# Kernel optimization log

Hardware: AMD Instinct MI355X
Metric: run time of the kernel (lower is better)

The kernel has to match this reference:

```python
import jax, jax.numpy as jnp
import numpy as np

DIM = 128       # pair channel dim
HID = 128       # orign_dim (projection dim)
N = 384         # sequence length (square pair map)
B = 1
EPS = 1e-5


def layer_norm(x, w, b):
    m = jnp.mean(x, axis=-1, keepdims=True)
    v = jnp.mean(jnp.square(x - m), axis=-1, keepdims=True)
    return (x - m) * jax.lax.rsqrt(v + EPS) * w + b


def setup_inputs() -> dict:
    key = jax.random.key(0)
    ks = jax.random.split(key, 16)
    s = 0.02
    return {
        "x": jax.random.normal(ks[0], (B, N, N, DIM), jnp.float32),
        "norm_w": jnp.ones((DIM,), jnp.float32),
        "norm_b": jnp.zeros((DIM,), jnp.float32),
        "left_w": jax.random.normal(ks[1], (HID, DIM), jnp.float32) * s,
        "left_b": jnp.zeros((HID,), jnp.float32),
        "right_w": jax.random.normal(ks[2], (HID, DIM), jnp.float32) * s,
        "right_b": jnp.zeros((HID,), jnp.float32),
        # gates: module inits weight=0, bias=1; use small random weights + bias 1
        # to keep the same math while exercising nontrivial values
        "lgate_w": jax.random.normal(ks[3], (HID, DIM), jnp.float32) * s,
        "lgate_b": jnp.ones((HID,), jnp.float32),
        "rgate_w": jax.random.normal(ks[4], (HID, DIM), jnp.float32) * s,
        "rgate_b": jnp.ones((HID,), jnp.float32),
        "ogate_w": jax.random.normal(ks[5], (HID, DIM), jnp.float32) * s,
        "ogate_b": jnp.ones((HID,), jnp.float32),
        "ton_w": jnp.ones((HID,), jnp.float32),
        "ton_b": jnp.zeros((HID,), jnp.float32),
        "out_w": jax.random.normal(ks[6], (DIM, HID), jnp.float32) * s,
        "out_b": jnp.zeros((DIM,), jnp.float32),
    }


def reference(x, norm_w, norm_b, left_w, left_b, right_w, right_b,
              lgate_w, lgate_b, rgate_w, rgate_b, ogate_w, ogate_b,
              ton_w, ton_b, out_w, out_b):
    xn = layer_norm(x, norm_w, norm_b)                       # [B,N,N,D]
    lin = lambda w, b: jnp.einsum('bijd,ed->bije', xn, w) + b
    left = lin(left_w, left_b) * jax.nn.sigmoid(lin(lgate_w, lgate_b))
    right = lin(right_w, right_b) * jax.nn.sigmoid(lin(rgate_w, rgate_b))
    out_gate = jax.nn.sigmoid(lin(ogate_w, ogate_b))
    # ingoing mix: '... k j d, ... k i d -> ... i j d'
    out = jnp.einsum('bkjd,bkid->bijd', left, right)         # [B,N,N,H]
    out = layer_norm(out, ton_w, ton_b)
    out = jnp.einsum('bijh,dh->bijd', out, out_w) + out_b
    return out * out_gate
```

## Files before the change

### kernel.cpp

```cpp
#include <hip/hip_runtime.h>
#include <stdint.h>

typedef unsigned short u16;
typedef short bf16x8 __attribute__((ext_vector_type(8)));
typedef short bf16x4 __attribute__((ext_vector_type(4)));
typedef float f32x4 __attribute__((ext_vector_type(4)));

#define NN 384
#define DIMC 128
#define NPOS (NN*NN)
#define EPSV 1e-5f
#define LNS 136

__device__ __forceinline__ u16 f2b(float f){
  union { float f; uint32_t u; } v; v.f = f;
  return (u16)((v.u + 0x7FFFu + ((v.u >> 16) & 1u)) >> 16);
}
__device__ __forceinline__ float b2f(u16 h){
  union { uint32_t u; float f; } v; v.u = ((uint32_t)h) << 16;
  return v.f;
}
__device__ __forceinline__ float sigm(float z){
  return __builtin_amdgcn_rcpf(1.0f + __expf(-z));
}

__device__ __forceinline__ void glds16(const u16* g, u16* l){
  __builtin_amdgcn_global_load_lds((const __attribute__((address_space(1))) void*)(g),
                                   (__attribute__((address_space(3))) void*)(l), 16, 0, 0);
}

__global__ void wconv_k(const float* __restrict__ s0, const float* __restrict__ s1,
                        const float* __restrict__ s2, const float* __restrict__ s3,
                        const float* __restrict__ s4, const float* __restrict__ s5,
                        u16* __restrict__ dst){
  int bid = blockIdx.x;
  int m = bid >> 6;
  int off = ((bid & 63) << 8) + threadIdx.x;
  const float* src = s0;
  if (m==1) src=s1; else if (m==2) src=s2; else if (m==3) src=s3;
  else if (m==4) src=s4; else if (m==5) src=s5;
  dst[(m<<14) + off] = f2b(src[off]);
}

__global__ __launch_bounds__(256) void proj_k(
    const float* __restrict__ x, const float* __restrict__ nw, const float* __restrict__ nb,
    const u16* __restrict__ wb,
    const float* __restrict__ left_b, const float* __restrict__ lgate_b,
    const float* __restrict__ right_b, const float* __restrict__ rgate_b,
    const float* __restrict__ ogate_b,
    u16* __restrict__ Lp, u16* __restrict__ Rp, u16* __restrict__ gate)
{
  __shared__ u16 xn[64*LNS];
  const int tid = threadIdx.x, lane = tid & 63, wid = tid >> 6;
  const int bid = blockIdx.x;
  const int c = bid % NN, r0 = (bid / NN) * 64;
  const int l15 = lane & 15, lg = lane >> 4;

  {
    float4 w0 = *(const float4*)(nw + l15*8);
    float4 w1 = *(const float4*)(nw + l15*8 + 4);
    float4 bb0 = *(const float4*)(nb + l15*8);
    float4 bb1 = *(const float4*)(nb + l15*8 + 4);
    #pragma unroll
    for (int it = 0; it < 4; ++it){
      int p = wid*16 + it*4 + lg;
      const float* xp = x + ((size_t)(r0 + p)*NN + c)*DIMC + l15*8;
      float4 v0 = *(const float4*)xp;
      float4 v1 = *(const float4*)(xp + 4);
      float s  = (v0.x+v0.y)+(v0.z+v0.w)+((v1.x+v1.y)+(v1.z+v1.w));
      float sq = v0.x*v0.x+v0.y*v0.y+v0.z*v0.z+v0.w*v0.w
               + v1.x*v1.x+v1.y*v1.y+v1.z*v1.z+v1.w*v1.w;
      #pragma unroll
      for (int o = 8; o; o >>= 1){ s += __shfl_xor(s, o); sq += __shfl_xor(sq, o); }
      float mean = s * (1.0f/128.0f);
      float var  = sq * (1.0f/128.0f) - mean*mean;
      float inv  = rsqrtf(var + EPSV);
      bf16x8 o8;
      o8[0] = (short)f2b((v0.x - mean)*inv*w0.x + bb0.x);
      o8[1] = (short)f2b((v0.y - mean)*inv*w0.y + bb0.y);
      o8[2] = (short)f2b((v0.z - mean)*inv*w0.z + bb0.z);
      o8[3] = (short)f2b((v0.w - mean)*inv*w0.w + bb0.w);
      o8[4] = (short)f2b((v1.x - mean)*inv*w1.x + bb1.x);
      o8[5] = (short)f2b((v1.y - mean)*inv*w1.y + bb1.y);
      o8[6] = (short)f2b((v1.z - mean)*inv*w1.z + bb1.z);
      o8[7] = (short)f2b((v1.w - mean)*inv*w1.w + bb1.w);
      *(bf16x8*)(xn + p*LNS + l15*8) = o8;
    }
  }
  __syncthreads();

  const int kofs = lg * 8;
  const int wrow = (wid*32 + l15) * 128;
  const int xrowbase = l15 * LNS;

  #pragma unroll
  for (int pr = 0; pr < 2; ++pr){
    const u16* wV = wb + (pr*2 + 0)*16384;
    const u16* wG = wb + (pr*2 + 1)*16384;
    const float* bV = pr ? right_b : left_b;
    const float* bG = pr ? rgate_b : lgate_b;
    u16* dst = pr ? Rp : Lp;

    f32x4 aV[2][4], aG[2][4];
    #pragma unroll
    for (int n = 0; n < 2; ++n)
      #pragma unroll
      for (int pt = 0; pt < 4; ++pt){ aV[n][pt] = {0.f,0.f,0.f,0.f}; aG[n][pt] = {0.f,0.f,0.f,0.f}; }

    #pragma unroll
    for (int ks = 0; ks < 4; ++ks){
      bf16x8 xf[4];
      #pragma unroll
      for (int pt = 0; pt < 4; ++pt)
        xf[pt] = *(const bf16x8*)(xn + xrowbase + pt*16*LNS + ks*32 + kofs);
      #pragma unroll
      for (int n = 0; n < 2; ++n){
        bf16x8 wv = *(const bf16x8*)(wV + wrow + n*16*128 + ks*32 + kofs);
        bf16x8 wg = *(const bf16x8*)(wG + wrow + n*16*128 + ks*32 + kofs);
        #pragma unroll
        for (int pt = 0; pt < 4; ++pt){
          aV[n][pt] = __builtin_amdgcn_mfma_f32_16x16x32_bf16(wv, xf[pt], aV[n][pt], 0, 0, 0);
          aG[n][pt] = __builtin_amdgcn_mfma_f32_16x16x32_bf16(wg, xf[pt], aG[n][pt], 0, 0, 0);
        }
      }
    }
    #pragma unroll
    for (int n = 0; n < 2; ++n){
      int ebase = wid*32 + n*16 + lg*4;
      float4 bv4 = *(const float4*)(bV + ebase);
      float4 bg4 = *(const float4*)(bG + ebase);
      #pragma unroll
      for (int r = 0; r < 4; ++r){
        float bv = r==0?bv4.x : r==1?bv4.y : r==2?bv4.z : bv4.w;
        float bg = r==0?bg4.x : r==1?bg4.y : r==2?bg4.z : bg4.w;
        u16* base = dst + (size_t)(ebase + r)*NPOS + (size_t)c*NN + r0 + l15;
        #pragma unroll
        for (int pt = 0; pt < 4; ++pt){
          float v = (aV[n][pt][r] + bv) * sigm(aG[n][pt][r] + bg);
          base[pt*16] = f2b(v);
        }
      }
    }
  }

  {
    const u16* wO = wb + 4*16384;
    f32x4 aO[2][4];
    #pragma unroll
    for (int n = 0; n < 2; ++n)
      #pragma unroll
      for (int pt = 0; pt < 4; ++pt) aO[n][pt] = {0.f,0.f,0.f,0.f};

    #pragma unroll
    for (int ks = 0; ks < 4; ++ks){
      bf16x8 xf[4];
      #pragma unroll
      for (int pt = 0; pt < 4; ++pt)
        xf[pt] = *(const bf16x8*)(xn + xrowbase + pt*16*LNS + ks*32 + kofs);
      #pragma unroll
      for (int n = 0; n < 2; ++n){
        bf16x8 wo = *(const bf16x8*)(wO + wrow + n*16*128 + ks*32 + kofs);
        #pragma unroll
        for (int pt = 0; pt < 4; ++pt)
          aO[n][pt] = __builtin_amdgcn_mfma_f32_16x16x32_bf16(wo, xf[pt], aO[n][pt], 0, 0, 0);
      }
    }
    __syncthreads();
    #pragma unroll
    for (int n = 0; n < 2; ++n){
      int ebase = wid*32 + n*16 + lg*4;
      float4 bo4 = *(const float4*)(ogate_b + ebase);
      #pragma unroll
      for (int r = 0; r < 4; ++r){
        float bo = r==0?bo4.x : r==1?bo4.y : r==2?bo4.z : bo4.w;
        #pragma unroll
        for (int pt = 0; pt < 4; ++pt)
          xn[(pt*16 + l15)*LNS + ebase + r] = f2b(sigm(aO[n][pt][r] + bo));
      }
    }
    __syncthreads();
    #pragma unroll
    for (int it = 0; it < 4; ++it){
      int idx = tid + it*256;
      int p = idx >> 4, s = idx & 15;
      *(bf16x8*)(gate + ((size_t)(r0 + p)*NN + c)*DIMC + s*8) = *(const bf16x8*)(xn + p*LNS + s*8);
    }
  }
}

__global__ __launch_bounds__(256) void phase2_k(const u16* __restrict__ Rp, const u16* __restrict__ Lp,
                                                u16* __restrict__ outp){
  __shared__ u16 lds[17408];
  u16* At = lds;
  u16* Bt = lds + 8192;
  const int tid = threadIdx.x, lane = tid & 63, wid = tid >> 6;
  const int bid = blockIdx.x;
  const int d = bid / 9, tile = bid % 9;
  const int i0 = (tile/3)*128, j0 = (tile%3)*128;
  const u16* Rb = Rp + (size_t)d*NPOS;
  const u16* Lb = Lp + (size_t)d*NPOS;
  const int wm = wid >> 1, wn = wid & 1;
  const int iw = wm*64, jw = wn*64;
  const int l15 = lane & 15, lg = lane >> 4;
  const int rmask = l15 & 7;

  int srcoff[4];
  #pragma unroll
  for (int c = 0; c < 4; ++c){
    int idx = wid*256 + c*64 + lane;
    int row = idx >> 3, slot = idx & 7;
    srcoff[c] = row*NN + ((slot ^ (row & 7)) * 8);
  }

  f32x4 acc[4][4];
  #pragma unroll
  for (int m = 0; m < 4; ++m)
    #pragma unroll
    for (int n = 0; n < 4; ++n) acc[m][n] = {0.f,0.f,0.f,0.f};

  const u16* Rt0 = Rb + (size_t)i0*NN;
  const u16* Lt0 = Lb + (size_t)j0*NN;

  for (int k0 = 0; k0 < NN; k0 += 64){
    __syncthreads();
    #pragma unroll
    for (int c = 0; c < 4; ++c){
      glds16(Rt0 + k0 + srcoff[c], At + (wid*4 + c)*512);
      glds16(Lt0 + k0 + srcoff[c], Bt + (wid*4 + c)*512);
    }
    asm volatile("s_waitcnt vmcnt(0)" ::: "memory");
    __syncthreads();
    #pragma unroll
    for (int ks = 0; ks < 2; ++ks){
      int sl = ((ks*4 + lg) ^ rmask) * 8;
      bf16x8 af[4], bfr[4];
      #pragma unroll
      for (int m = 0; m < 4; ++m)
        af[m] = *(const bf16x8*)(At + (iw + m*16 + l15)*64 + sl);
      #pragma unroll
      for (int n = 0; n < 4; ++n)
        bfr[n] = *(const bf16x8*)(Bt + (jw + n*16 + l15)*64 + sl);
      #pragma unroll
      for (int m = 0; m < 4; ++m)
        #pragma unroll
        for (int n = 0; n < 4; ++n)
          acc[m][n] = __builtin_amdgcn_mfma_f32_16x16x32_bf16(af[m], bfr[n], acc[m][n], 0, 0, 0);
    }
  }

  __syncthreads();
  #pragma unroll
  for (int m = 0; m < 4; ++m)
    #pragma unroll
    for (int n = 0; n < 4; ++n)
      #pragma unroll
      for (int r = 0; r < 4; ++r)
        lds[(iw + m*16 + lg*4 + r)*136 + jw + n*16 + l15] = f2b(acc[m][n][r]);
  __syncthreads();
  u16* ob = outp + (size_t)d*NPOS;
  #pragma unroll
  for (int it = 0; it < 8; ++it){
    int idx = tid + it*256;
    int i = idx >> 4, s = idx & 15;
    *(bf16x8*)(ob + (size_t)(i0 + i)*NN + j0 + s*8) = *(const bf16x8*)(lds + i*136 + s*8);
  }
}

__global__ __launch_bounds__(256) void phase3_k(const u16* __restrict__ outp,
    const float* __restrict__ tonw, const float* __restrict__ tonb,
    const u16* __restrict__ wOut, const float* __restrict__ out_b,
    const u16* __restrict__ gate, float* __restrict__ out)
{
  __shared__ u16 xn2[64*132];
  __shared__ float reds[4][64], redq[4][64];
  __shared__ float marr[64], iarr[64];
  const int tid = threadIdx.x, lane = tid & 63, wid = tid >> 6;
  const int bid = blockIdx.x;
  const int i = bid % NN, j0 = (bid / NN) * 64;
  const int l15 = lane & 15, lg = lane >> 4;

  float rv[32];
  float s = 0.f, sq = 0.f;
  #pragma unroll
  for (int q = 0; q < 32; ++q){
    int h = wid*32 + q;
    float v = b2f(outp[(size_t)h*NPOS + (size_t)i*NN + j0 + lane]);
    rv[q] = v; s += v; sq += v*v;
  }
  reds[wid][lane] = s; redq[wid][lane] = sq;
  __syncthreads();
  if (tid < 64){
    float ts = reds[0][tid] + reds[1][tid] + reds[2][tid] + reds[3][tid];
    float tq = redq[0][tid] + redq[1][tid] + redq[2][tid] + redq[3][tid];
    float m  = ts * (1.f/128.f);
    float var = tq * (1.f/128.f) - m*m;
    marr[tid] = m; iarr[tid] = rsqrtf(var + EPSV);
  }
  __syncthreads();
  float m = marr[lane], inv = iarr[lane];
  #pragma unroll
  for (int q = 0; q < 32; ++q){
    int h = wid*32 + q;
    float v = (rv[q] - m)*inv*tonw[h] + tonb[h];
    xn2[lane*132 + h] = f2b(v);
  }
  __syncthreads();

  f32x4 acc[8];
  #pragma unroll
  for (int n = 0; n < 8; ++n) acc[n] = {0.f,0.f,0.f,0.f};
  const int row = wid*16 + l15;
  const int kofs = lg * 8;
  #pragma unroll
  for (int ks = 0; ks < 4; ++ks){
    const u16* ap = xn2 + row*132 + ks*32 + kofs;
    bf16x4 a0 = *(const bf16x4*)ap;
    bf16x4 a1 = *(const bf16x4*)(ap + 4);
    bf16x8 af = __builtin_shufflevector(a0, a1, 0,1,2,3,4,5,6,7);
    #pragma unroll
    for (int n = 0; n < 8; ++n){
      bf16x8 bm = *(const bf16x8*)(wOut + (n*16 + l15)*128 + ks*32 + kofs);
      acc[n] = __builtin_amdgcn_mfma_f32_16x16x32_bf16(af, bm, acc[n], 0, 0, 0);
    }
  }
  #pragma unroll
  for (int n = 0; n < 8; ++n){
    int dd = n*16 + l15;
    float bo = out_b[dd];
    #pragma unroll
    for (int r = 0; r < 4; ++r){
      int p = wid*16 + lg*4 + r;
      size_t base = ((size_t)i*NN + j0 + p)*DIMC + dd;
      float g = b2f(gate[base]);
      out[base] = (acc[n][r] + bo) * g;
    }
  }
}

extern "C" void kernel_launch(void* const* d_in, const int* in_sizes, int n_in,
                              void* d_out, int out_size, void* d_ws, size_t ws_size,
                              hipStream_t stream){
  const float* x       = (const float*)d_in[0];
  const float* norm_w  = (const float*)d_in[1];
  const float* norm_b  = (const float*)d_in[2];
  const float* left_w  = (const float*)d_in[3];
  const float* left_b  = (const float*)d_in[4];
  const float* right_w = (const float*)d_in[5];
  const float* right_b = (const float*)d_in[6];
  const float* lgate_w = (const float*)d_in[7];
  const float* lgate_b = (const float*)d_in[8];
  const float* rgate_w = (const float*)d_in[9];
  const float* rgate_b = (const float*)d_in[10];
  const float* ogate_w = (const float*)d_in[11];
  const float* ogate_b = (const float*)d_in[12];
  const float* ton_w   = (const float*)d_in[13];
  const float* ton_b   = (const float*)d_in[14];
  const float* out_w   = (const float*)d_in[15];
  const float* out_b   = (const float*)d_in[16];

  char* ws = (char*)d_ws;
  const size_t SZ = (size_t)NPOS * DIMC * sizeof(u16);
  u16* Lp   = (u16*)(ws);
  u16* Rp   = (u16*)(ws + SZ);
  u16* gate = (u16*)(ws + 2*SZ);
  u16* outp = (u16*)(ws + 3*SZ);
  u16* wb   = (u16*)(ws + 4*SZ);

  wconv_k<<<dim3(384), dim3(256), 0, stream>>>(left_w, lgate_w, right_w, rgate_w, ogate_w, out_w, wb);
  proj_k<<<dim3(2304), dim3(256), 0, stream>>>(x, norm_w, norm_b, wb,
      left_b, lgate_b, right_b, rgate_b, ogate_b, Lp, Rp, gate);
  phase2_k<<<dim3(1152), dim3(256), 0, stream>>>(Rp, Lp, outp);
  phase3_k<<<dim3(2304), dim3(256), 0, stream>>>(outp, ton_w, ton_b, wb + 5*16384, out_b, gate, (float*)d_out);
}
```

Measured before the change: 175.9 us.

## Double-buffer phase2 LDS loads and split proj accumulators to cut registers

The batched-matmul phase2 kernel now uses 32-wide K tiles in two LDS buffers, with a new XOR swizzle. It prefetches the next tile with global_load_lds while MFMAs run on the current one, waiting only for the older loads. The aim is to hide global-load latency that the old load-wait-compute loop exposed. Separately, proj_k processes its 64-position tile in two halves with fewer live accumulators and adds a launch bound of 4 blocks per CU to raise occupancy. The risks are more barriers per K step in phase2 and possible register spills in proj_k.

```diff
diff --git a/kernel.cpp b/kernel.cpp
--- a/kernel.cpp
+++ b/kernel.cpp
@@ -42,7 +42,7 @@
   dst[(m<<14) + off] = f2b(src[off]);
 }
 
-__global__ __launch_bounds__(256) void proj_k(
+__global__ __launch_bounds__(256, 4) void proj_k(
     const float* __restrict__ x, const float* __restrict__ nw, const float* __restrict__ nb,
     const u16* __restrict__ wb,
     const float* __restrict__ left_b, const float* __restrict__ lgate_b,
@@ -101,43 +101,46 @@
     const float* bG = pr ? rgate_b : lgate_b;
     u16* dst = pr ? Rp : Lp;
 
-    f32x4 aV[2][4], aG[2][4];
-    #pragma unroll
-    for (int n = 0; n < 2; ++n)
-      #pragma unroll
-      for (int pt = 0; pt < 4; ++pt){ aV[n][pt] = {0.f,0.f,0.f,0.f}; aG[n][pt] = {0.f,0.f,0.f,0.f}; }
-
-    #pragma unroll
-    for (int ks = 0; ks < 4; ++ks){
-      bf16x8 xf[4];
-      #pragma unroll
-      for (int pt = 0; pt < 4; ++pt)
-        xf[pt] = *(const bf16x8*)(xn + xrowbase + pt*16*LNS + ks*32 + kofs);
-      #pragma unroll
-      for (int n = 0; n < 2; ++n){
-        bf16x8 wv = *(const bf16x8*)(wV + wrow + n*16*128 + ks*32 + kofs);
-        bf16x8 wg = *(const bf16x8*)(wG + wrow + n*16*128 + ks*32 + kofs);
-        #pragma unroll
-        for (int pt = 0; pt < 4; ++pt){
-          aV[n][pt] = __builtin_amdgcn_mfma_f32_16x16x32_bf16(wv, xf[pt], aV[n][pt], 0, 0, 0);
-          aG[n][pt] = __builtin_amdgcn_mfma_f32_16x16x32_bf16(wg, xf[pt], aG[n][pt], 0, 0, 0);
+    #pragma unroll
+    for (int h = 0; h < 2; ++h){
+      f32x4 aV[2][2], aG[2][2];
+      #pragma unroll
+      for (int n = 0; n < 2; ++n)
+        #pragma unroll
+        for (int q = 0; q < 2; ++q){ aV[n][q] = {0.f,0.f,0.f,0.f}; aG[n][q] = {0.f,0.f,0.f,0.f}; }
+
+      #pragma unroll
+      for (int ks = 0; ks < 4; ++ks){
+        bf16x8 xf[2];
+        #pragma unroll
+        for (int q = 0; q < 2; ++q)
+          xf[q] = *(const bf16x8*)(xn + xrowbase + (h*2 + q)*16*LNS + ks*32 + kofs);
+        #pragma unroll
+        for (int n = 0; n < 2; ++n){
+          bf16x8 wv = *(const bf16x8*)(wV + wrow + n*16*128 + ks*32 + kofs);
+          bf16x8 wg = *(const bf16x8*)(wG + wrow + n*16*128 + ks*32 + kofs);
+          #pragma unroll
+          for (int q = 0; q < 2; ++q){
+            aV[n][q] = __builtin_amdgcn_mfma_f32_16x16x32_bf16(wv, xf[q], aV[n][q], 0, 0, 0);
+            aG[n][q] = __builtin_amdgcn_mfma_f32_16x16x32_bf16(wg, xf[q], aG[n][q], 0, 0, 0);
+          }
         }
       }
-    }
-    #pragma unroll
-    for (int n = 0; n < 2; ++n){
-      int ebase = wid*32 + n*16 + lg*4;
-      float4 bv4 = *(const float4*)(bV + ebase);
-      float4 bg4 = *(const float4*)(bG + ebase);
-      #pragma unroll
-      for (int r = 0; r < 4; ++r){
-        float bv = r==0?bv4.x : r==1?bv4.y : r==2?bv4.z : bv4.w;
-        float bg = r==0?bg4.x : r==1?bg4.y : r==2?bg4.z : bg4.w;
-        u16* base = dst + (size_t)(ebase + r)*NPOS + (size_t)c*NN + r0 + l15;
-        #pragma unroll
-        for (int pt = 0; pt < 4; ++pt){
-          float v = (aV[n][pt][r] + bv) * sigm(aG[n][pt][r] + bg);
-          base[pt*16] = f2b(v);
+      #pragma unroll
+      for (int n = 0; n < 2; ++n){
+        int ebase = wid*32 + n*16 + lg*4;
+        float4 bv4 = *(const float4*)(bV + ebase);
+        float4 bg4 = *(const float4*)(bG + ebase);
+        #pragma unroll
+        for (int r = 0; r < 4; ++r){
+          float bv = r==0?bv4.x : r==1?bv4.y : r==2?bv4.z : bv4.w;
+          float bg = r==0?bg4.x : r==1?bg4.y : r==2?bg4.z : bg4.w;
+          u16* base = dst + (size_t)(ebase + r)*NPOS + (size_t)c*NN + r0 + l15;
+          #pragma unroll
+          for (int q = 0; q < 2; ++q){
+            float v = (aV[n][q][r] + bv) * sigm(aG[n][q][r] + bg);
+            base[(h*2 + q)*16] = f2b(v);
+          }
         }
       }
     }
@@ -191,26 +194,27 @@
 __global__ __launch_bounds__(256) void phase2_k(const u16* __restrict__ Rp, const u16* __restrict__ Lp,
                                                 u16* __restrict__ outp){
   __shared__ u16 lds[17408];
-  u16* At = lds;
-  u16* Bt = lds + 8192;
   const int tid = threadIdx.x, lane = tid & 63, wid = tid >> 6;
   const int bid = blockIdx.x;
   const int d = bid / 9, tile = bid % 9;
   const int i0 = (tile/3)*128, j0 = (tile%3)*128;
-  const u16* Rb = Rp + (size_t)d*NPOS;
-  const u16* Lb = Lp + (size_t)d*NPOS;
   const int wm = wid >> 1, wn = wid & 1;
   const int iw = wm*64, jw = wn*64;
   const int l15 = lane & 15, lg = lane >> 4;
-  const int rmask = l15 & 7;
-
-  int srcoff[4];
-  #pragma unroll
-  for (int c = 0; c < 4; ++c){
-    int idx = wid*256 + c*64 + lane;
-    int row = idx >> 3, slot = idx & 7;
-    srcoff[c] = row*NN + ((slot ^ (row & 7)) * 8);
-  }
+
+  const u16* Rt0 = Rp + (size_t)d*NPOS + (size_t)i0*NN;
+  const u16* Lt0 = Lp + (size_t)d*NPOS + (size_t)j0*NN;
+
+  int soff[2];
+  #pragma unroll
+  for (int cc = 0; cc < 2; ++cc){
+    int idx = cc*256 + tid;
+    int row = idx >> 2, slot = idx & 3;
+    soff[cc] = row*NN + ((slot ^ ((row >> 1) & 3)) * 8);
+  }
+  const int db0 = (wid*64)*8;
+  const int db1 = (256 + wid*64)*8;
+  const int rsw = ((lg ^ ((l15 >> 1) & 3)) * 8);
 
   f32x4 acc[4][4];
   #pragma unroll
@@ -218,37 +222,42 @@
     #pragma unroll
     for (int n = 0; n < 4; ++n) acc[m][n] = {0.f,0.f,0.f,0.f};
 
-  const u16* Rt0 = Rb + (size_t)i0*NN;
-  const u16* Lt0 = Lb + (size_t)j0*NN;
-
-  for (int k0 = 0; k0 < NN; k0 += 64){
+  glds16(Rt0 + soff[0], lds + db0);
+  glds16(Rt0 + soff[1], lds + db1);
+  glds16(Lt0 + soff[0], lds + 8192 + db0);
+  glds16(Lt0 + soff[1], lds + 8192 + db1);
+
+  for (int t = 0; t < 12; ++t){
+    u16* Acur = lds + (t & 1)*4096;
+    u16* Bcur = lds + 8192 + (t & 1)*4096;
+    if (t < 11){
+      u16* Anx = lds + ((t+1) & 1)*4096;
+      u16* Bnx = lds + 8192 + ((t+1) & 1)*4096;
+      int k = (t+1)*32;
+      glds16(Rt0 + k + soff[0], Anx + db0);
+      glds16(Rt0 + k + soff[1], Anx + db1);
+      glds16(Lt0 + k + soff[0], Bnx + db0);
+      glds16(Lt0 + k + soff[1], Bnx + db1);
+      asm volatile("s_waitcnt vmcnt(4)" ::: "memory");
+    } else {
+      asm volatile("s_waitcnt vmcnt(0)" ::: "memory");
+    }
     __syncthreads();
-    #pragma unroll
-    for (int c = 0; c < 4; ++c){
-      glds16(Rt0 + k0 + srcoff[c], At + (wid*4 + c)*512);
-      glds16(Lt0 + k0 + srcoff[c], Bt + (wid*4 + c)*512);
-    }
-    asm volatile("s_waitcnt vmcnt(0)" ::: "memory");
+    bf16x8 af[4], bfr[4];
+    #pragma unroll
+    for (int m = 0; m < 4; ++m)
+      af[m] = *(const bf16x8*)(Acur + (iw + m*16 + l15)*32 + rsw);
+    #pragma unroll
+    for (int n = 0; n < 4; ++n)
+      bfr[n] = *(const bf16x8*)(Bcur + (jw + n*16 + l15)*32 + rsw);
+    #pragma unroll
+    for (int m = 0; m < 4; ++m)
+      #pragma unroll
+      for (int n = 0; n < 4; ++n)
+        acc[m][n] = __builtin_amdgcn_mfma_f32_16x16x32_bf16(af[m], bfr[n], acc[m][n], 0, 0, 0);
     __syncthreads();
-    #pragma unroll
-    for (int ks = 0; ks < 2; ++ks){
-      int sl = ((ks*4 + lg) ^ rmask) * 8;
-      bf16x8 af[4], bfr[4];
-      #pragma unroll
-      for (int m = 0; m < 4; ++m)
-        af[m] = *(const bf16x8*)(At + (iw + m*16 + l15)*64 + sl);
-      #pragma unroll
-      for (int n = 0; n < 4; ++n)
-        bfr[n] = *(const bf16x8*)(Bt + (jw + n*16 + l15)*64 + sl);
-      #pragma unroll
-      for (int m = 0; m < 4; ++m)
-        #pragma unroll
-        for (int n = 0; n < 4; ++n)
-          acc[m][n] = __builtin_amdgcn_mfma_f32_16x16x32_bf16(af[m], bfr[n], acc[m][n], 0, 0, 0);
-    }
-  }
-
-  __syncthreads();
+  }
+
   #pragma unroll
   for (int m = 0; m < 4; ++m)
     #pragma unroll
```

Measured after the change: 222.6 us. 26.5% more time.
